# Optimization experiments

Measured on AMD Instinct MI355X. Metric: run time of the kernel, lower is better.

## Reference

```python
import jax, jax.numpy as jnp
import numpy as np

DIM = 1024
NUM_HEADS = 8  # only used for the scale; heads are never actually split
SCALE = float((DIM // NUM_HEADS) ** 0.5)


def _attn(x, wq, wk, wv):
    # Single-head full-dim attention, faithful to the source (no head split).
    Q = x @ wq.T  # [B,S,D]
    K = x @ wk.T
    V = x @ wv.T
    scores = jnp.einsum('bqd,bkd->bqk', Q, K) / SCALE  # [B,S,S]
    attn = jax.nn.softmax(scores, axis=-1)
    return jnp.einsum('bqk,bkd->bqd', attn, V)


def setup_inputs() -> dict:
    key = jax.random.key(0)
    ks = jax.random.split(key, 9)
    B, S, D = 4, 2048, DIM
    w = lambda k: jax.random.normal(k, (D, D), dtype=jnp.float32) * 0.02
    return {
        'x': jax.random.normal(ks[0], (B, S, D), dtype=jnp.float32),
        'wq1': w(ks[1]), 'wk1': w(ks[2]), 'wv1': w(ks[3]),
        'fc1_w': w(ks[4]),
        'wq2': w(ks[5]), 'wk2': w(ks[6]), 'wv2': w(ks[7]),
        'fc2_w': w(ks[8]),
    }


def reference(x, wq1, wk1, wv1, fc1_w, wq2, wk2, wv2, fc2_w):
    h = _attn(x, wq1, wk1, wv1)
    h = jax.nn.silu(h)
    h = h @ fc1_w.T
    h = _attn(h, wq2, wk2, wv2)
    h = jax.nn.silu(h)
    h = h @ fc2_w.T
    return jax.nn.softmax(h, axis=-1)
```

## Files before the change

kernel.cpp:

```cpp
#include <hip/hip_runtime.h>
#include <math.h>


typedef __attribute__((ext_vector_type(8))) int i32x8;
typedef __attribute__((ext_vector_type(4))) int i32x4;
typedef __attribute__((ext_vector_type(4))) float f32x4;
typedef unsigned char u8;
typedef unsigned int u32;

#define EPI_F8 1
#define EPI_RV 2
#define EPI_EXP 3
#define EPI_PV 4
#define EPI_EXPF32 5

__device__ __forceinline__ void gload_lds16(const void* g, void* l) {
    __builtin_amdgcn_global_load_lds(
        (const __attribute__((address_space(1))) void*)g,
        (__attribute__((address_space(3))) void*)l, 16, 0, 0);
}

__device__ __forceinline__ u8 cvt_f8(float v) {
    return (u8)(__builtin_amdgcn_cvt_pk_fp8_f32(v, v, 0, false) & 0xFF);
}

__device__ __forceinline__ u32 pack_f8x4(float v0, float v1, float v2, float v3) {
    int p01 = __builtin_amdgcn_cvt_pk_fp8_f32(v0, v1, 0, false);
    int p23 = __builtin_amdgcn_cvt_pk_fp8_f32(v2, v3, 0, false);
    return (u32)(p01 & 0xFFFF) | ((u32)p23 << 16);
}

#define MFMA_F8(a, b, c) \
    __builtin_amdgcn_mfma_scale_f32_16x16x128_f8f6f4( \
        (a), (b), (c), 0, 0, 0, 0x7F7F7F7F, 0, 0x7F7F7F7F)

template <int EPI>
__global__ __launch_bounds__(256) void gemm_fp8(
    const u8* __restrict__ A, const u8* __restrict__ B,
    void* __restrict__ C0, void* __restrict__ C1, void* __restrict__ C2,
    int K, int ldA, int ldB, int ldC,
    long long bsA, long long bsB, long long bsC, float alpha, float beta)
{
    __shared__ u8 sA[128 * 128];
    __shared__ u8 sB[128 * 128];

    const int tid = threadIdx.x;
    const int wave = tid >> 6, lane = tid & 63;
    const int wm = wave >> 1, wn = wave & 1;
    const int m0 = blockIdx.y * 128, n0 = blockIdx.x * 128;
    const long long z = blockIdx.z;

    const u8* pA = A + z * bsA;
    const u8* pB = B + z * bsB;

    int blkid[4], rs_[4], cs16[4];
#pragma unroll
    for (int i = 0; i < 4; i++) {
        blkid[i] = wave * 256 + i * 64 + lane;
        rs_[i] = blkid[i] >> 3;
        cs16[i] = ((blkid[i] & 7) ^ (rs_[i] & 7)) * 16;
    }

    f32x4 acc[4][4] = {};
    const int fr = lane & 15, fc2 = (lane >> 4) * 2;

    for (int k0 = 0; k0 < K; k0 += 128) {
#pragma unroll
        for (int i = 0; i < 4; i++) {
            gload_lds16(pA + (long long)(m0 + rs_[i]) * ldA + k0 + cs16[i],
                        sA + blkid[i] * 16);
            gload_lds16(pB + (long long)(n0 + rs_[i]) * ldB + k0 + cs16[i],
                        sB + blkid[i] * 16);
        }
        __syncthreads();

        i32x8 a[4], b[4];
#pragma unroll
        for (int i = 0; i < 4; i++) {
            const int row = wm * 64 + i * 16 + fr;
            const int sw = row & 7;
            i32x4 lo = *(const i32x4*)(sA + row * 128 + ((fc2 + 0) ^ sw) * 16);
            i32x4 hi = *(const i32x4*)(sA + row * 128 + ((fc2 + 1) ^ sw) * 16);
            a[i] = __builtin_shufflevector(lo, hi, 0, 1, 2, 3, 4, 5, 6, 7);
        }
#pragma unroll
        for (int j = 0; j < 4; j++) {
            const int row = wn * 64 + j * 16 + fr;
            const int sw = row & 7;
            i32x4 lo = *(const i32x4*)(sB + row * 128 + ((fc2 + 0) ^ sw) * 16);
            i32x4 hi = *(const i32x4*)(sB + row * 128 + ((fc2 + 1) ^ sw) * 16);
            b[j] = __builtin_shufflevector(lo, hi, 0, 1, 2, 3, 4, 5, 6, 7);
        }
#pragma unroll
        for (int i = 0; i < 4; i++)
#pragma unroll
            for (int j = 0; j < 4; j++)
                acc[i][j] = MFMA_F8(a[i], b[j], acc[i][j]);
        __syncthreads();
    }

    const int col = lane & 15;
    const int rbase = (lane >> 4) * 4;

    if (EPI == EPI_F8) {
#pragma unroll
        for (int j = 0; j < 4; j++) {
            const int Cq = n0 + wn * 64 + j * 16 + col;
#pragma unroll
            for (int i = 0; i < 4; i++) {
                const int R0 = m0 + wm * 64 + i * 16 + rbase;
                u8* C = (u8*)C0 + z * bsC;
                *(u32*)(C + (long long)Cq * ldC + R0) =
                    pack_f8x4(acc[i][j][0] * alpha, acc[i][j][1] * alpha,
                              acc[i][j][2] * alpha, acc[i][j][3] * alpha);
            }
        }
    }
    (void)beta; (void)C1; (void)C2;
}

template <int EPI>
__global__ __launch_bounds__(512, 4) void gemm64(
    const u8* __restrict__ A, const u8* __restrict__ B,
    void* __restrict__ C0, void* __restrict__ C1, void* __restrict__ C2,
    int K, int ldA, int ldB, int ldC,
    long long bsA, long long bsB, long long bsC, float alpha, float beta)
{
    __shared__ __align__(16) u8 sA[2][64 * 128];
    __shared__ __align__(16) u8 sB[2][256 * 128];

    const int tid = threadIdx.x;
    const int wave = tid >> 6, lane = tid & 63;
    const int m0 = blockIdx.y * 64, n0 = blockIdx.x * 256;
    const long long z = blockIdx.z;

    const u8* pA = A + z * bsA;
    const u8* pB = B + z * bsB;

    const int rA = tid >> 3;
    const long long offA = (long long)(m0 + rA) * ldA +
                           (((tid & 7) ^ (rA & 7)) * 16);
    const int dstA = tid * 16;
    long long offB[4];
    int dstB[4];
#pragma unroll
    for (int l = 0; l < 4; l++) {
        const int id = l * 512 + tid;
        const int r = id >> 3, c = (id & 7) ^ (r & 7);
        offB[l] = (long long)(n0 + r) * ldB + c * 16;
        dstB[l] = id * 16;
    }

    f32x4 acc[4][2] = {};
    const int fr = lane & 15, fc2 = (lane >> 4) * 2;
    const int NT = K >> 7;

    auto STAGE = [&](int t) {
        const long long kb = (long long)t << 7;
        const int buf = t & 1;
        gload_lds16(pA + offA + kb, &sA[buf][dstA]);
#pragma unroll
        for (int l = 0; l < 4; l++)
            gload_lds16(pB + offB[l] + kb, &sB[buf][dstB[l]]);
    };

    STAGE(0);
    __syncthreads();

    for (int t = 0; t < NT; ++t) {
        if (t + 1 < NT) STAGE(t + 1);

        const int buf = t & 1;
        i32x8 a[4], b[2];
#pragma unroll
        for (int i = 0; i < 4; i++) {
            const int row = i * 16 + fr;
            const int sw = row & 7;
            const u8* p = &sA[buf][row * 128];
            i32x4 lo = *(const i32x4*)(p + ((fc2 + 0) ^ sw) * 16);
            i32x4 hi = *(const i32x4*)(p + ((fc2 + 1) ^ sw) * 16);
            a[i] = __builtin_shufflevector(lo, hi, 0, 1, 2, 3, 4, 5, 6, 7);
        }
#pragma unroll
        for (int j = 0; j < 2; j++) {
            const int row = wave * 32 + j * 16 + fr;
            const int sw = row & 7;
            const u8* p = &sB[buf][row * 128];
            i32x4 lo = *(const i32x4*)(p + ((fc2 + 0) ^ sw) * 16);
            i32x4 hi = *(const i32x4*)(p + ((fc2 + 1) ^ sw) * 16);
            b[j] = __builtin_shufflevector(lo, hi, 0, 1, 2, 3, 4, 5, 6, 7);
        }
#pragma unroll
        for (int i = 0; i < 4; i++)
#pragma unroll
            for (int j = 0; j < 2; j++)
                acc[i][j] = MFMA_F8(a[i], b[j], acc[i][j]);

        __syncthreads();
    }

    const int col = lane & 15;
    const int rbase = (lane >> 4) * 4;

    if (EPI == EPI_EXP) {
        u8* P = (u8*)C0 + z * bsC;
        float* rsum = (float*)C1 + z * 2048;
#pragma unroll
        for (int j = 0; j < 2; j++) {
            const int Cq = n0 + wave * 32 + j * 16 + col;
            float part = 0.f;
#pragma unroll
            for (int i = 0; i < 4; i++) {
                const int R0 = m0 + i * 16 + rbase;
                float e0 = __expf(acc[i][j][0] * alpha);
                float e1 = __expf(acc[i][j][1] * alpha);
                float e2 = __expf(acc[i][j][2] * alpha);
                float e3 = __expf(acc[i][j][3] * alpha);
                part += (e0 + e1) + (e2 + e3);
                *(u32*)(P + (long long)Cq * ldC + R0) =
                    pack_f8x4(e0 * 0.0625f, e1 * 0.0625f,
                              e2 * 0.0625f, e3 * 0.0625f);
            }
            part += __shfl_xor(part, 16);
            part += __shfl_xor(part, 32);
            if (lane < 16) atomicAdd(&rsum[Cq], part);
        }
        return;
    }

    if (EPI == EPI_EXPF32) {
        float* Cw = (float*)C0;
        float* rsum = (float*)C1;
#pragma unroll
        for (int j = 0; j < 2; j++) {
            const int Cq = n0 + wave * 32 + j * 16 + col;
            float part = 0.f;
#pragma unroll
            for (int i = 0; i < 4; i++) {
                const int R0 = m0 + i * 16 + rbase;
                float4 e;
                e.x = __expf(acc[i][j][0] * alpha);
                e.y = __expf(acc[i][j][1] * alpha);
                e.z = __expf(acc[i][j][2] * alpha);
                e.w = __expf(acc[i][j][3] * alpha);
                part += (e.x + e.y) + (e.z + e.w);
                *(float4*)(Cw + (long long)Cq * ldC + R0) = e;
            }
            part += __shfl_xor(part, 16);
            part += __shfl_xor(part, 32);
            if (lane < 16) atomicAdd(&rsum[Cq], part);
        }
        return;
    }

#pragma unroll
    for (int j = 0; j < 2; j++) {
        const int Cq = n0 + wave * 32 + j * 16 + col;
        float inv;
        if (EPI == EPI_PV) {
            const float* rsum = (const float*)C1 + z * 2048;
            inv = alpha / rsum[Cq];
        }
#pragma unroll
        for (int i = 0; i < 4; i++) {
            const int R0 = m0 + i * 16 + rbase;
            if (EPI == EPI_F8) {
                u8* C = (u8*)C0 + z * bsC;
                *(u32*)(C + (long long)Cq * ldC + R0) =
                    pack_f8x4(acc[i][j][0] * alpha, acc[i][j][1] * alpha,
                              acc[i][j][2] * alpha, acc[i][j][3] * alpha);
            } else if (EPI == EPI_PV) {
                u8* C = (u8*)C0 + z * bsC;
                float v[4];
#pragma unroll
                for (int r = 0; r < 4; r++) {
                    float t = acc[i][j][r] * inv;
                    v[r] = (t / (1.f + __expf(-t))) * beta;
                }
                *(u32*)(C + (long long)Cq * ldC + R0) =
                    pack_f8x4(v[0], v[1], v[2], v[3]);
            } else {
                const int seg = R0 >> 10;
                const int db = R0 & 1023;
                if (seg == 1) {
                    const int bb = Cq >> 11, tt = Cq & 2047;
                    u8* VTp = (u8*)C2;
#pragma unroll
                    for (int r = 0; r < 4; r++)
                        VTp[(long long)bb * (1024LL * 2048) +
                            (long long)(db + r) * 2048 + tt] =
                            cvt_f8(acc[i][j][r] * beta);
                } else {
                    u8* C = (u8*)C0;
                    *(u32*)(C + (long long)Cq * 1024 + db) =
                        pack_f8x4(acc[i][j][0] * alpha, acc[i][j][1] * alpha,
                                  acc[i][j][2] * alpha, acc[i][j][3] * alpha);
                }
            }
        }
    }
}

__global__ __launch_bounds__(256) void convert_all(
    const float* x, const float* wv1, const float* wv2, const float* fc1,
    const float* fc2, u8* __restrict__ ax, u8* __restrict__ bproj,
    u8* __restrict__ wfc, float* __restrict__ rz)
{
    const int bid = blockIdx.x;
    if (bid < 24) {
        float4 zero = {0.f, 0.f, 0.f, 0.f};
        *(float4*)(rz + ((long long)bid * 256 + threadIdx.x) * 4) = zero;
    }
    const float* src;
    u8* dst;
    float scale;
    long long i;
    if (bid < 8192) {
        src = x; dst = ax; scale = 8.f;
        i = ((long long)bid * 256 + threadIdx.x) * 4;
    } else {
        const int idx = bid - 8192;
        const int wi = idx >> 10;
        const float* srcs[4] = {wv1, wv2, fc1, fc2};
        u8* dsts[4] = {bproj + (1 << 20), bproj + 3 * (1 << 20),
                       wfc, wfc + (1 << 20)};
        src = srcs[wi]; dst = dsts[wi]; scale = 256.f;
        i = (((long long)(idx & 1023)) * 256 + threadIdx.x) * 4;
    }
    float4 v = *(const float4*)(src + i);
    *(u32*)(dst + i) = pack_f8x4(v.x * scale, v.y * scale,
                                 v.z * scale, v.w * scale);
}

__global__ __launch_bounds__(256) void convert_t(
    const float* wq1, const float* wk1, const float* wq2, const float* wk2,
    u8* __restrict__ o)
{
    const float* srcs[4] = {wq1, wk1, wq2, wk2};
    const float* src = srcs[blockIdx.y];
    u8* dst = o + (long long)blockIdx.y * (1 << 20);
    const int q0 = (blockIdx.x & 15) * 64, d0 = (blockIdx.x >> 4) * 64;
    const int qq = (threadIdx.x & 15) * 4, dd = (threadIdx.x >> 4) * 4;
    float4 v[4];
#pragma unroll
    for (int s = 0; s < 4; s++)
        v[s] = *(const float4*)(src + (long long)(q0 + qq + s) * 1024 + d0 + dd);
    const float* vf = (const float*)v;
#pragma unroll
    for (int r = 0; r < 4; r++)
        *(u32*)(dst + (long long)(d0 + dd + r) * 1024 + q0 + qq) =
            pack_f8x4(vf[0 * 4 + r] * 256.f, vf[1 * 4 + r] * 256.f,
                      vf[2 * 4 + r] * 256.f, vf[3 * 4 + r] * 256.f);
}

__global__ __launch_bounds__(256) void normalize_1024(
    const float* __restrict__ e, const float* __restrict__ rsum,
    float* __restrict__ out)
{
    const long long row = blockIdx.x;
    const float inv = 1.0f / rsum[row];
    const float* p = e + row * 1024;
    float* o = out + row * 1024;
    float4 v = *(const float4*)(p + threadIdx.x * 4);
    float4 ov;
    ov.x = v.x * inv; ov.y = v.y * inv; ov.z = v.z * inv; ov.w = v.w * inv;
    *(float4*)(o + threadIdx.x * 4) = ov;
}

extern "C" void kernel_launch(void* const* d_in, const int* in_sizes, int n_in,
                              void* d_out, int out_size, void* d_ws, size_t ws_size,
                              hipStream_t stream)
{
    float* out = (float*)d_out;

    constexpr int Bt = 4, S = 2048, D = 1024;
    constexpr int M = Bt * S;
    const long long MD = (long long)M * D;
    const long long DD = (long long)D * D;
    const long long SD = (long long)S * D;
    const long long SS = (long long)S * S;

    u8* Af = (u8*)d_ws;
    u8* Bproj = Af + MD;
    u8* WqT = Bproj + 2 * 2048 * 1024;
    u8* Wfc = WqT + 4 * DD;
    u8* Rf = Wfc + 2 * DD;
    u8* VT = Rf + MD;
    u8* Pf = VT + MD;
    u8* Hs = Pf + (long long)Bt * SS;
    float* SC = (float*)(Hs + MD);
    float* rsum0 = SC + MD;
    float* rsum1 = rsum0 + M;
    float* rsum2 = rsum1 + M;

    const dim3 blk(256);
    const dim3 blk2(512);

    const float SOFT = 0.08838834764831845f;
    const float a_d1   = 1.f / 64.f;
    const float a_R[2] = {1.f / 512.f, 1.f / 1024.f};
    const float b_V[2] = {1.f / 256.f, 1.f / 64.f};
    const float a_qk[2] = {SOFT / 128.f, SOFT / 65536.f};
    const float a_pv[2] = {2.0f, 1.f / 64.f};
    const float b_pv[2] = {256.f, 65536.f};
    const float a_fc[2] = {256.f / 65536.f, 1.f / 16777216.f};

    convert_all<<<dim3(12288), blk, 0, stream>>>(
        (const float*)d_in[0], (const float*)d_in[3], (const float*)d_in[7],
        (const float*)d_in[4], (const float*)d_in[8], Af, Bproj, Wfc, rsum0);
    convert_t<<<dim3(256, 4), blk, 0, stream>>>(
        (const float*)d_in[1], (const float*)d_in[2], (const float*)d_in[5],
        (const float*)d_in[6], WqT);
    gemm_fp8<EPI_F8><<<dim3(8, 8, 2), blk, 0, stream>>>(
        WqT, WqT + DD, Bproj, nullptr, nullptr, D, D, D, D,
        2 * DD, 2 * DD, (long long)2048 * 1024, a_d1, 0.f);

    const dim3 grv(M / 256, 2048 / 64, 1);
    const dim3 gqk(S / 256, S / 64, Bt);
    const dim3 gpv(S / 256, D / 64, Bt);
    const dim3 gw(M / 256, D / 64, 1);

    for (int layer = 0; layer < 2; layer++) {
        const u8* bp = Bproj + (long long)layer * 2048 * 1024;
        const u8* fc = Wfc + (long long)layer * DD;
        float* rsum = layer ? rsum1 : rsum0;

        gemm64<EPI_RV><<<grv, blk2, 0, stream>>>(
            bp, Af, Rf, nullptr, VT, D, D, D, D, 0, 0, 0,
            a_R[layer], b_V[layer]);
        gemm64<EPI_EXP><<<gqk, blk2, 0, stream>>>(
            Af, Rf, Pf, rsum, nullptr, D, D, D, S, SD, SD, SS,
            a_qk[layer], 0.f);
        gemm64<EPI_PV><<<gpv, blk2, 0, stream>>>(
            VT, Pf, Hs, rsum, nullptr, S, S, S, D,
            (long long)D * S, SS, SD, a_pv[layer], b_pv[layer]);
        if (layer == 0) {
            gemm64<EPI_F8><<<gw, blk2, 0, stream>>>(
                fc, Hs, Af, nullptr, nullptr, D, D, D, D, 0, 0, 0,
                a_fc[0], 0.f);
        } else {
            gemm64<EPI_EXPF32><<<gw, blk2, 0, stream>>>(
                fc, Hs, SC, rsum2, nullptr, D, D, D, D, 0, 0, 0,
                a_fc[1], 0.f);
        }
    }

    normalize_1024<<<dim3(M), blk, 0, stream>>>(SC, rsum2, out);
}
```

Measured before the change: 341.8 us.

## Shrink gemm64 tile to 64x128 with 256 threads and triple-buffered LDS pipeline

The main FP8 GEMM kernel moves from a 512-thread 64x256 tile to a 256-thread 64x128 tile. Its LDS staging goes from double to triple buffering: loads run two k-steps ahead and are waited on with explicit vmcnt counts and raw barriers instead of __syncthreads. The aim is to hide global-to-LDS latency better and to launch more blocks, which should improve occupancy and load balance. In exchange each block reuses less of the A tile, more blocks re-read the same data, and the hand-written waitcnt logic must match the number of loads issued.

```diff
diff --git a/kernel.cpp b/kernel.cpp
--- a/kernel.cpp
+++ b/kernel.cpp
@@ -120,32 +120,35 @@
 }
 
 template <int EPI>
-__global__ __launch_bounds__(512, 4) void gemm64(
+__global__ __launch_bounds__(256, 2) void gemm64t(
     const u8* __restrict__ A, const u8* __restrict__ B,
     void* __restrict__ C0, void* __restrict__ C1, void* __restrict__ C2,
     int K, int ldA, int ldB, int ldC,
     long long bsA, long long bsB, long long bsC, float alpha, float beta)
 {
-    __shared__ __align__(16) u8 sA[2][64 * 128];
-    __shared__ __align__(16) u8 sB[2][256 * 128];
+    __shared__ __align__(16) u8 sA[3][64 * 128];
+    __shared__ __align__(16) u8 sB[3][128 * 128];
 
     const int tid = threadIdx.x;
     const int wave = tid >> 6, lane = tid & 63;
-    const int m0 = blockIdx.y * 64, n0 = blockIdx.x * 256;
+    const int m0 = blockIdx.y * 64, n0 = blockIdx.x * 128;
     const long long z = blockIdx.z;
 
     const u8* pA = A + z * bsA;
     const u8* pB = B + z * bsB;
 
-    const int rA = tid >> 3;
-    const long long offA = (long long)(m0 + rA) * ldA +
-                           (((tid & 7) ^ (rA & 7)) * 16);
-    const int dstA = tid * 16;
-    long long offB[4];
-    int dstB[4];
+    long long offA[2]; int dstA[2];
+#pragma unroll
+    for (int l = 0; l < 2; l++) {
+        const int id = l * 256 + tid;
+        const int r = id >> 3, c = (id & 7) ^ (r & 7);
+        offA[l] = (long long)(m0 + r) * ldA + c * 16;
+        dstA[l] = id * 16;
+    }
+    long long offB[4]; int dstB[4];
 #pragma unroll
     for (int l = 0; l < 4; l++) {
-        const int id = l * 512 + tid;
+        const int id = l * 256 + tid;
         const int r = id >> 3, c = (id & 7) ^ (r & 7);
         offB[l] = (long long)(n0 + r) * ldB + c * 16;
         dstB[l] = id * 16;
@@ -157,20 +160,26 @@
 
     auto STAGE = [&](int t) {
         const long long kb = (long long)t << 7;
-        const int buf = t & 1;
-        gload_lds16(pA + offA + kb, &sA[buf][dstA]);
+        const int buf = t % 3;
+#pragma unroll
+        for (int l = 0; l < 2; l++)
+            gload_lds16(pA + offA[l] + kb, &sA[buf][dstA[l]]);
 #pragma unroll
         for (int l = 0; l < 4; l++)
             gload_lds16(pB + offB[l] + kb, &sB[buf][dstB[l]]);
     };
 
     STAGE(0);
-    __syncthreads();
+    STAGE(1);
+    asm volatile("s_waitcnt vmcnt(6)" ::: "memory");
+    __builtin_amdgcn_sched_barrier(0);
+    __builtin_amdgcn_s_barrier();
+    __builtin_amdgcn_sched_barrier(0);
 
     for (int t = 0; t < NT; ++t) {
-        if (t + 1 < NT) STAGE(t + 1);
-
-        const int buf = t & 1;
+        if (t + 2 < NT) STAGE(t + 2);
+
+        const int buf = t % 3;
         i32x8 a[4], b[2];
 #pragma unroll
         for (int i = 0; i < 4; i++) {
@@ -196,7 +205,13 @@
             for (int j = 0; j < 2; j++)
                 acc[i][j] = MFMA_F8(a[i], b[j], acc[i][j]);
 
-        __syncthreads();
+        if (t + 2 < NT)
+            asm volatile("s_waitcnt vmcnt(6)" ::: "memory");
+        else
+            asm volatile("s_waitcnt vmcnt(0)" ::: "memory");
+        __builtin_amdgcn_sched_barrier(0);
+        __builtin_amdgcn_s_barrier();
+        __builtin_amdgcn_sched_barrier(0);
     }
 
     const int col = lane & 15;
@@ -394,7 +409,6 @@
     float* rsum2 = rsum1 + M;
 
     const dim3 blk(256);
-    const dim3 blk2(512);
 
     const float SOFT = 0.08838834764831845f;
     const float a_d1   = 1.f / 64.f;
@@ -415,31 +429,31 @@
         WqT, WqT + DD, Bproj, nullptr, nullptr, D, D, D, D,
         2 * DD, 2 * DD, (long long)2048 * 1024, a_d1, 0.f);
 
-    const dim3 grv(M / 256, 2048 / 64, 1);
-    const dim3 gqk(S / 256, S / 64, Bt);
-    const dim3 gpv(S / 256, D / 64, Bt);
-    const dim3 gw(M / 256, D / 64, 1);
+    const dim3 grv(M / 128, 2048 / 64, 1);
+    const dim3 gqk(S / 128, S / 64, Bt);
+    const dim3 gpv(S / 128, D / 64, Bt);
+    const dim3 gw(M / 128, D / 64, 1);
 
     for (int layer = 0; layer < 2; layer++) {
         const u8* bp = Bproj + (long long)layer * 2048 * 1024;
         const u8* fc = Wfc + (long long)layer * DD;
         float* rsum = layer ? rsum1 : rsum0;
 
-        gemm64<EPI_RV><<<grv, blk2, 0, stream>>>(
+        gemm64t<EPI_RV><<<grv, blk, 0, stream>>>(
             bp, Af, Rf, nullptr, VT, D, D, D, D, 0, 0, 0,
             a_R[layer], b_V[layer]);
-        gemm64<EPI_EXP><<<gqk, blk2, 0, stream>>>(
+        gemm64t<EPI_EXP><<<gqk, blk, 0, stream>>>(
             Af, Rf, Pf, rsum, nullptr, D, D, D, S, SD, SD, SS,
             a_qk[layer], 0.f);
-        gemm64<EPI_PV><<<gpv, blk2, 0, stream>>>(
+        gemm64t<EPI_PV><<<gpv, blk, 0, stream>>>(
             VT, Pf, Hs, rsum, nullptr, S, S, S, D,
             (long long)D * S, SS, SD, a_pv[layer], b_pv[layer]);
         if (layer == 0) {
-            gemm64<EPI_F8><<<gw, blk2, 0, stream>>>(
+            gemm64t<EPI_F8><<<gw, blk, 0, stream>>>(
                 fc, Hs, Af, nullptr, nullptr, D, D, D, D, 0, 0, 0,
                 a_fc[0], 0.f);
         } else {
-            gemm64<EPI_EXPF32><<<gw, blk2, 0, stream>>>(
+            gemm64t<EPI_EXPF32><<<gw, blk, 0, stream>>>(
                 fc, Hs, SC, rsum2, nullptr, D, D, D, D, 0, 0, 0,
                 a_fc[1], 0.f);
         }
```

Result: slower. 394.2 us (+15.3%).
